# Performance work log

Hardware: AMD Instinct MI355X
Metric: run time of the kernel (lower is better)

## Reference

```python
import jax, jax.numpy as jnp
import numpy as np

N = 100000
E = 1600000
F_IN = 256
HEADS = 8
C1 = 8
NCLS = 16
NEG_SLOPE = 0.2


def setup_inputs() -> dict:
    key = jax.random.key(0)
    ks = jax.random.split(key, 8)
    x = jax.random.normal(ks[0], (N, F_IN), dtype=jnp.float32)
    edge_index = jax.random.randint(ks[1], (2, E), 0, N, dtype=jnp.int64)
    W1 = jax.random.normal(ks[2], (F_IN, HEADS * C1), dtype=jnp.float32) * (1.0 / np.sqrt(F_IN))
    a1_src = jax.random.normal(ks[3], (HEADS, C1), dtype=jnp.float32) * 0.1
    a1_dst = jax.random.normal(ks[4], (HEADS, C1), dtype=jnp.float32) * 0.1
    b1 = jnp.zeros((HEADS * C1,), dtype=jnp.float32)
    W2 = jax.random.normal(ks[5], (HEADS * C1, NCLS), dtype=jnp.float32) * (1.0 / np.sqrt(HEADS * C1))
    a2_src = jax.random.normal(ks[6], (1, NCLS), dtype=jnp.float32) * 0.1
    a2_dst = jax.random.normal(ks[7], (1, NCLS), dtype=jnp.float32) * 0.1
    b2 = jnp.zeros((NCLS,), dtype=jnp.float32)
    return {"x": x, "edge_index": edge_index, "W1": W1, "a1_src": a1_src,
            "a1_dst": a1_dst, "b1": b1, "W2": W2, "a2_src": a2_src,
            "a2_dst": a2_dst, "b2": b2}


def gat_layer(x, src, dst, W, a_src, a_dst, b, heads, out_c, concat):
    n = x.shape[0]
    h = (x @ W).reshape(n, heads, out_c)            # [N,H,C]
    al_src = (h * a_src).sum(-1)                    # [N,H]
    al_dst = (h * a_dst).sum(-1)                    # [N,H]
    e = jax.nn.leaky_relu(al_src[src] + al_dst[dst], NEG_SLOPE)  # [E',H]
    m = jax.ops.segment_max(e, dst, num_segments=n)              # per-dst max
    alpha = jnp.exp(e - m[dst])
    denom = jax.ops.segment_sum(alpha, dst, num_segments=n)
    alpha = alpha / denom[dst]
    out = jax.ops.segment_sum(h[src] * alpha[:, :, None], dst, num_segments=n)  # [N,H,C]
    out = out.reshape(n, heads * out_c) if concat else out.mean(axis=1)
    return out + b


def reference(x, edge_index, W1, a1_src, a1_dst, b1, W2, a2_src, a2_dst, b2):
    # add self-loops (PyG GATConv default)
    loop = jnp.arange(N, dtype=edge_index.dtype)
    src = jnp.concatenate([edge_index[0], loop])
    dst = jnp.concatenate([edge_index[1], loop])
    # dropout layers are identity in eval mode
    h = jax.nn.elu(gat_layer(x, src, dst, W1, a1_src, a1_dst, b1, HEADS, C1, True))
    out = gat_layer(h, src, dst, W2, a2_src, a2_dst, b2, 1, NCLS, False)
    return jax.nn.log_softmax(out, axis=-1)
```

## Files before the change

### kernel.cpp

```cpp
#include <hip/hip_runtime.h>
#include <math.h>

#define NN   100000
#define EE   1600000
#define FIN  256
#define NCLS 16
#define NEG  0.2f

#define NEDGE (EE + NN)
#define WBKT  256
#define NBKT  ((NN + WBKT - 1) / WBKT)
#define CAP   5120
#define ABLK  4096
#define NABLK ((NEDGE + ABLK - 1) / ABLK)
#define NGBLK ((NN + 63) / 64)

#define OFF_GCNT  0
#define OFF_BASE  392
#define OFF_ROW   784
#define OFF_BKT   100788
#define OFF_ADJ   (OFF_BKT + NBKT*CAP)
#define OFF_H1B   (OFF_ADJ + NEDGE)
#define OFF_H1E   (OFF_H1B + NN*32)
#define OFF_AL1S  (OFF_H1E + NN*32)
#define OFF_AL1D  (OFF_AL1S + NN*8)
#define OFF_H2B   (OFF_AL1D + NN*8)
#define OFF_AL2S  (OFF_H2B + NN*8)
#define OFF_AL2D  (OFF_AL2S + NN)

__device__ __forceinline__ float lrelu(float x) { return x >= 0.f ? x : NEG * x; }
__device__ __forceinline__ unsigned short f2bf(float x) {
    unsigned u = __float_as_uint(x);
    return (unsigned short)((u + 0x7FFF + ((u >> 16) & 1)) >> 16);
}
__device__ __forceinline__ float bf2f(unsigned short b) {
    return __uint_as_float(((unsigned)b) << 16);
}
__device__ __forceinline__ float bflo(unsigned u) { return __uint_as_float(u << 16); }
__device__ __forceinline__ float bfhi(unsigned u) { return __uint_as_float(u & 0xFFFF0000u); }

__global__ __launch_bounds__(256) void k_binA_gemm1(
    const int* __restrict__ esrc, const int* __restrict__ edst,
    int* __restrict__ gcnt, unsigned* __restrict__ bkt,
    const float* __restrict__ x, const float* __restrict__ W1,
    const float* __restrict__ a1s, const float* __restrict__ a1d,
    unsigned short* __restrict__ h1b, float* __restrict__ al1s, float* __restrict__ al1d)
{
    const int t = threadIdx.x;
    if (blockIdx.x < NABLK) {
        __shared__ int lcnt[NBKT];
        __shared__ int lbase[NBKT];
        const int e0 = blockIdx.x * ABLK;
        for (int i = t; i < NBKT; i += 256) lcnt[i] = 0;
        __syncthreads();

        unsigned wrd[16];
        unsigned short bb[16], ll[16];
        #pragma unroll
        for (int j = 0; j < 16; ++j) {
            int ei = e0 + j * 256 + t;
            bb[j] = 0xFFFFu;
            if (ei < NEDGE) {
                int s, d;
                if (ei < EE) { s = esrc[ei]; d = edst[ei]; } else { s = d = ei - EE; }
                int b = d >> 8;
                wrd[j] = ((unsigned)s << 8) | (unsigned)(d & 255);
                bb[j] = (unsigned short)b;
                ll[j] = (unsigned short)atomicAdd(&lcnt[b], 1);
            }
        }
        __syncthreads();
        for (int i = t; i < NBKT; i += 256)
            lbase[i] = lcnt[i] ? atomicAdd(&gcnt[i], lcnt[i]) : 0;
        __syncthreads();
        #pragma unroll
        for (int j = 0; j < 16; ++j) {
            if (bb[j] != 0xFFFFu) {
                int b = bb[j];
                bkt[(size_t)b * CAP + lbase[b] + ll[j]] = wrd[j];
            }
        }
        return;
    }

    __shared__ float sxT[32][68];
    __shared__ float sW[32][64];
    const int n0 = (blockIdx.x - NABLK) * 64;
    const int tr = t >> 4, tc = t & 15;

    const int xr0 = t >> 3,         xf0 = t & 7;
    const int xr1 = (t + 256) >> 3, xf1 = (t + 256) & 7;
    const int wr0 = t >> 4,         wf0 = t & 15;
    const int wr1 = (t + 256) >> 4, wf1 = (t + 256) & 15;
    const int nx0 = n0 + xr0, nx1 = n0 + xr1;

    float acc[4][4] = {};
    float4 px0, px1, pw0, pw1;

    px0 = (nx0 < NN) ? *(const float4*)(x + (size_t)nx0 * FIN + xf0 * 4)
                     : make_float4(0.f, 0.f, 0.f, 0.f);
    px1 = (nx1 < NN) ? *(const float4*)(x + (size_t)nx1 * FIN + xf1 * 4)
                     : make_float4(0.f, 0.f, 0.f, 0.f);
    pw0 = *(const float4*)(W1 + (size_t)wr0 * 64 + wf0 * 4);
    pw1 = *(const float4*)(W1 + (size_t)wr1 * 64 + wf1 * 4);

    for (int kc = 0; kc < 256; kc += 32) {
        __syncthreads();
        sxT[xf0 * 4 + 0][xr0] = px0.x;
        sxT[xf0 * 4 + 1][xr0] = px0.y;
        sxT[xf0 * 4 + 2][xr0] = px0.z;
        sxT[xf0 * 4 + 3][xr0] = px0.w;
        sxT[xf1 * 4 + 0][xr1] = px1.x;
        sxT[xf1 * 4 + 1][xr1] = px1.y;
        sxT[xf1 * 4 + 2][xr1] = px1.z;
        sxT[xf1 * 4 + 3][xr1] = px1.w;
        *(float4*)&sW[wr0][wf0 * 4] = pw0;
        *(float4*)&sW[wr1][wf1 * 4] = pw1;
        __syncthreads();

        if (kc + 32 < 256) {
            int kn = kc + 32;
            px0 = (nx0 < NN) ? *(const float4*)(x + (size_t)nx0 * FIN + kn + xf0 * 4)
                             : make_float4(0.f, 0.f, 0.f, 0.f);
            px1 = (nx1 < NN) ? *(const float4*)(x + (size_t)nx1 * FIN + kn + xf1 * 4)
                             : make_float4(0.f, 0.f, 0.f, 0.f);
            pw0 = *(const float4*)(W1 + (size_t)(kn + wr0) * 64 + wf0 * 4);
            pw1 = *(const float4*)(W1 + (size_t)(kn + wr1) * 64 + wf1 * 4);
        }

        #pragma unroll
        for (int k = 0; k < 32; ++k) {
            float4 a = *(const float4*)&sxT[k][tr * 4];
            float4 b = *(const float4*)&sW[k][tc * 4];
            acc[0][0] += a.x * b.x; acc[0][1] += a.x * b.y; acc[0][2] += a.x * b.z; acc[0][3] += a.x * b.w;
            acc[1][0] += a.y * b.x; acc[1][1] += a.y * b.y; acc[1][2] += a.y * b.z; acc[1][3] += a.y * b.w;
            acc[2][0] += a.z * b.x; acc[2][1] += a.z * b.y; acc[2][2] += a.z * b.z; acc[2][3] += a.z * b.w;
            acc[3][0] += a.w * b.x; acc[3][1] += a.w * b.y; acc[3][2] += a.w * b.z; acc[3][3] += a.w * b.w;
        }
    }

    #pragma unroll
    for (int j = 0; j < 4; ++j) {
        int n = n0 + tr * 4 + j;
        if (n < NN) {
            ushort4 v = make_ushort4(f2bf(acc[j][0]), f2bf(acc[j][1]), f2bf(acc[j][2]), f2bf(acc[j][3]));
            *(ushort4*)(h1b + (size_t)n * 64 + tc * 4) = v;
        }
    }

    float sa[4], da[4];
    #pragma unroll
    for (int u = 0; u < 4; ++u) { sa[u] = a1s[tc * 4 + u]; da[u] = a1d[tc * 4 + u]; }
    #pragma unroll
    for (int j = 0; j < 4; ++j) {
        float vs = acc[j][0] * sa[0] + acc[j][1] * sa[1] + acc[j][2] * sa[2] + acc[j][3] * sa[3];
        float vd = acc[j][0] * da[0] + acc[j][1] * da[1] + acc[j][2] * da[2] + acc[j][3] * da[3];
        vs += __shfl_xor(vs, 1, 64);
        vd += __shfl_xor(vd, 1, 64);
        int n = n0 + tr * 4 + j;
        if (!(tc & 1) && n < NN) {
            al1s[n * 8 + (tc >> 1)] = vs;
            al1d[n * 8 + (tc >> 1)] = vd;
        }
    }
}

__global__ __launch_bounds__(512) void k_scanB(
    const int* __restrict__ gcnt, int* __restrict__ base, int* __restrict__ row)
{
    __shared__ int s[512];
    int t = threadIdx.x;
    int v = (t < NBKT) ? gcnt[t] : 0;
    s[t] = v;
    __syncthreads();
    for (int off = 1; off < 512; off <<= 1) {
        int u = (t >= off) ? s[t - off] : 0;
        __syncthreads();
        s[t] += u;
        __syncthreads();
    }
    if (t <= NBKT) base[t] = s[t] - v;
    if (t == 0) row[NN] = NEDGE;
}

__global__ __launch_bounds__(256) void k_binC(
    const int* __restrict__ gcnt, const int* __restrict__ base,
    const unsigned* __restrict__ bkt, int* __restrict__ row, int* __restrict__ adj)
{
    __shared__ unsigned wd[CAP];
    __shared__ int hist[256], pref[256], cnt2[256];
    const int g = blockIdx.x, t = threadIdx.x;
    const int cn = gcnt[g], bs = base[g];
    hist[t] = 0; cnt2[t] = 0;
    __syncthreads();
    for (int i = t; i < cn; i += 256) {
        unsigned w = bkt[(size_t)g * CAP + i];
        wd[i] = w;
        atomicAdd(&hist[w & 255], 1);
    }
    __syncthreads();
    int v = hist[t];
    pref[t] = v;
    __syncthreads();
    for (int off = 1; off < 256; off <<= 1) {
        int u = (t >= off) ? pref[t - off] : 0;
        __syncthreads();
        pref[t] += u;
        __syncthreads();
    }
    int ex = pref[t] - v;
    int n = g * 256 + t;
    if (n < NN) row[n] = bs + ex;
    pref[t] = ex;
    __syncthreads();
    for (int i = t; i < cn; i += 256) {
        unsigned w = wd[i];
        int dl = w & 255;
        int p = atomicAdd(&cnt2[dl], 1);
        adj[bs + pref[dl] + p] = (int)(w >> 8);
    }
}

__global__ __launch_bounds__(256) void k_agg1(
    const int* __restrict__ row, const int* __restrict__ adj,
    const float* __restrict__ al1s, const float* __restrict__ al1d,
    const unsigned* __restrict__ h1b2, const float* __restrict__ b1,
    unsigned* __restrict__ h1e2)
{
    const int wv = threadIdx.x >> 6, lane = threadIdx.x & 63;
    const int n = blockIdx.x * 4 + wv;
    const int q = lane >> 4;
    const int r = lane & 15;
    const int h = r >> 1;
    const float ald = al1d[n * 8 + h];
    const int r0 = row[n], r1 = row[n + 1];

    float dsum = 0.f, ax = 0.f, ay = 0.f, bx = 0.f, by = 0.f;
    for (int c0 = r0; c0 < r1; c0 += 64) {
        int li = c0 + lane;
        int adjv = adj[li < r1 ? li : r0];
        int m = r1 - c0; if (m > 64) m = 64;
        int k = 0;
        for (; k + 16 <= m; k += 16) {
            int s0 = __shfl(adjv, k + 0  + q, 64);
            int s1 = __shfl(adjv, k + 4  + q, 64);
            int s2 = __shfl(adjv, k + 8  + q, 64);
            int s3 = __shfl(adjv, k + 12 + q, 64);
            float a0 = al1s[s0 * 8 + h];
            float a1 = al1s[s1 * 8 + h];
            float a2 = al1s[s2 * 8 + h];
            float a3 = al1s[s3 * 8 + h];
            uint2 u0 = *(const uint2*)(h1b2 + s0 * 32 + r * 2);
            uint2 u1 = *(const uint2*)(h1b2 + s1 * 32 + r * 2);
            uint2 u2 = *(const uint2*)(h1b2 + s2 * 32 + r * 2);
            uint2 u3 = *(const uint2*)(h1b2 + s3 * 32 + r * 2);
            float w0 = __expf(lrelu(a0 + ald));
            float w1 = __expf(lrelu(a1 + ald));
            float w2 = __expf(lrelu(a2 + ald));
            float w3 = __expf(lrelu(a3 + ald));
            dsum += (w0 + w1) + (w2 + w3);
            ax += w0 * bflo(u0.x) + w1 * bflo(u1.x) + w2 * bflo(u2.x) + w3 * bflo(u3.x);
            ay += w0 * bfhi(u0.x) + w1 * bfhi(u1.x) + w2 * bfhi(u2.x) + w3 * bfhi(u3.x);
            bx += w0 * bflo(u0.y) + w1 * bflo(u1.y) + w2 * bflo(u2.y) + w3 * bflo(u3.y);
            by += w0 * bfhi(u0.y) + w1 * bfhi(u1.y) + w2 * bfhi(u2.y) + w3 * bfhi(u3.y);
        }
        for (; k < m; k += 4) {
            int kk = k + q;
            bool act = kk < m;
            int s0 = __shfl(adjv, act ? kk : 0, 64);
            float w0 = act ? __expf(lrelu(al1s[s0 * 8 + h] + ald)) : 0.f;
            uint2 u0 = *(const uint2*)(h1b2 + s0 * 32 + r * 2);
            dsum += w0;
            ax += w0 * bflo(u0.x);
            ay += w0 * bfhi(u0.x);
            bx += w0 * bflo(u0.y);
            by += w0 * bfhi(u0.y);
        }
    }
    dsum += __shfl_xor(dsum, 16, 64); dsum += __shfl_xor(dsum, 32, 64);
    ax   += __shfl_xor(ax,   16, 64); ax   += __shfl_xor(ax,   32, 64);
    ay   += __shfl_xor(ay,   16, 64); ay   += __shfl_xor(ay,   32, 64);
    bx   += __shfl_xor(bx,   16, 64); bx   += __shfl_xor(bx,   32, 64);
    by   += __shfl_xor(by,   16, 64); by   += __shfl_xor(by,   32, 64);

    float inv = 1.f / dsum;
    float v0 = ax * inv + b1[r * 4 + 0];
    float v1 = ay * inv + b1[r * 4 + 1];
    float v2 = bx * inv + b1[r * 4 + 2];
    float v3 = by * inv + b1[r * 4 + 3];
    v0 = v0 > 0.f ? v0 : __expf(v0) - 1.f;
    v1 = v1 > 0.f ? v1 : __expf(v1) - 1.f;
    v2 = v2 > 0.f ? v2 : __expf(v2) - 1.f;
    v3 = v3 > 0.f ? v3 : __expf(v3) - 1.f;
    if (q == 0) {
        uint2 o;
        o.x = (unsigned)f2bf(v0) | ((unsigned)f2bf(v1) << 16);
        o.y = (unsigned)f2bf(v2) | ((unsigned)f2bf(v3) << 16);
        *(uint2*)(h1e2 + n * 32 + r * 2) = o;
    }
}

__global__ __launch_bounds__(256) void k_gemm2(
    const unsigned short* __restrict__ h1e, const float* __restrict__ W2,
    const float* __restrict__ a2s, const float* __restrict__ a2d,
    unsigned short* __restrict__ h2b, float* __restrict__ al2s, float* __restrict__ al2d)
{
    __shared__ float sW[64 * 16];
    const int t = threadIdx.x;
    for (int i = t; i < 64 * 16; i += 256) sW[i] = W2[i];
    __syncthreads();
    const int n = blockIdx.x * 16 + (t >> 4);
    const int k = t & 15;
    if (n >= NN) return;
    const unsigned short* hr = h1e + (size_t)n * 64;
    float acc = 0.f;
    #pragma unroll
    for (int c = 0; c < 64; ++c) acc += bf2f(hr[c]) * sW[c * 16 + k];
    h2b[(size_t)n * 16 + k] = f2bf(acc);
    float vs = acc * a2s[k], vd = acc * a2d[k];
    #pragma unroll
    for (int off = 1; off < 16; off <<= 1) {
        vs += __shfl_xor(vs, off, 64);
        vd += __shfl_xor(vd, off, 64);
    }
    if (k == 0) { al2s[n] = vs; al2d[n] = vd; }
}

__global__ __launch_bounds__(256) void k_agg2(
    const int* __restrict__ row, const int* __restrict__ adj,
    const float* __restrict__ al2s, const float* __restrict__ al2d,
    const unsigned* __restrict__ h2b2, const float* __restrict__ b2,
    float* __restrict__ out)
{
    const int wv = threadIdx.x >> 6, lane = threadIdx.x & 63;
    const int n = blockIdx.x * 4 + wv;
    const float ald = al2d[n];
    const int r0 = row[n], r1 = row[n + 1];

    const int j = lane >> 2;
    const int r = lane & 3;
    float dsum = 0.f, ax = 0.f, ay = 0.f, bx = 0.f, by = 0.f;
    for (int i = r0; i < r1; i += 16) {
        int i0 = i + j;
        bool act = i0 < r1;
        int s = adj[act ? i0 : r0];
        float w = act ? __expf(lrelu(al2s[s] + ald)) : 0.f;
        uint2 u = *(const uint2*)(h2b2 + s * 8 + r * 2);
        dsum += w;
        ax += w * bflo(u.x);
        ay += w * bfhi(u.x);
        bx += w * bflo(u.y);
        by += w * bfhi(u.y);
    }
    #pragma unroll
    for (int off = 4; off < 64; off <<= 1) {
        dsum += __shfl_xor(dsum, off, 64);
        ax   += __shfl_xor(ax,   off, 64);
        ay   += __shfl_xor(ay,   off, 64);
        bx   += __shfl_xor(bx,   off, 64);
        by   += __shfl_xor(by,   off, 64);
    }
    float inv = 1.f / dsum;
    float v0 = ax * inv + b2[r * 4 + 0];
    float v1 = ay * inv + b2[r * 4 + 1];
    float v2 = bx * inv + b2[r * 4 + 2];
    float v3 = by * inv + b2[r * 4 + 3];

    float mx = fmaxf(fmaxf(v0, v1), fmaxf(v2, v3));
    mx = fmaxf(mx, __shfl_xor(mx, 1, 64));
    mx = fmaxf(mx, __shfl_xor(mx, 2, 64));
    float se = __expf(v0 - mx) + __expf(v1 - mx) + __expf(v2 - mx) + __expf(v3 - mx);
    se += __shfl_xor(se, 1, 64);
    se += __shfl_xor(se, 2, 64);
    float ls = mx + __logf(se);
    if (j == 0)
        *(float4*)(out + (size_t)n * 16 + r * 4) = make_float4(v0 - ls, v1 - ls, v2 - ls, v3 - ls);
}

extern "C" void kernel_launch(void* const* d_in, const int* in_sizes, int n_in,
                              void* d_out, int out_size, void* d_ws, size_t ws_size,
                              hipStream_t stream)
{
    const float* x    = (const float*)d_in[0];
    const int*   eidx = (const int*)d_in[1];
    const float* W1   = (const float*)d_in[2];
    const float* a1s  = (const float*)d_in[3];
    const float* a1d  = (const float*)d_in[4];
    const float* b1   = (const float*)d_in[5];
    const float* W2   = (const float*)d_in[6];
    const float* a2s  = (const float*)d_in[7];
    const float* a2d  = (const float*)d_in[8];
    const float* b2   = (const float*)d_in[9];
    float* out = (float*)d_out;
    float* ws  = (float*)d_ws;

    const int* esrc = eidx;
    const int* edst = eidx + EE;

    int* gcnt = (int*)(ws + OFF_GCNT);
    int* base = (int*)(ws + OFF_BASE);
    int* row  = (int*)(ws + OFF_ROW);
    unsigned* bkt = (unsigned*)(ws + OFF_BKT);
    int* adj  = (int*)(ws + OFF_ADJ);
    unsigned short* h1b = (unsigned short*)(ws + OFF_H1B);
    unsigned short* h1e = (unsigned short*)(ws + OFF_H1E);
    float* al1s  = ws + OFF_AL1S;
    float* al1d  = ws + OFF_AL1D;
    unsigned short* h2b = (unsigned short*)(ws + OFF_H2B);
    float* al2s  = ws + OFF_AL2S;
    float* al2d  = ws + OFF_AL2D;

    hipMemsetAsync(gcnt, 0, 392 * sizeof(int), stream);

    k_binA_gemm1<<<NABLK + NGBLK, 256, 0, stream>>>(esrc, edst, gcnt, bkt,
                                                    x, W1, a1s, a1d, h1b, al1s, al1d);
    k_scanB<<<1,    512, 0, stream>>>(gcnt, base, row);
    k_binC <<<NBKT, 256, 0, stream>>>(gcnt, base, bkt, row, adj);

    k_agg1 <<<NN / 4, 256, 0, stream>>>(row, adj, al1s, al1d, (const unsigned*)h1b, b1, (unsigned*)h1e);
    k_gemm2<<<NN / 16, 256, 0, stream>>>(h1e, W2, a2s, a2d, h2b, al2s, al2d);
    k_agg2 <<<NN / 4, 256, 0, stream>>>(row, adj, al2s, al2d, (const unsigned*)h2b, b2, out);
}
```

Measured before the change: 355.3 us.

## Split gemm1 blocks across binning kernels and stage gemm2 inputs in LDS

The layer-1 GEMM blocks are split so that some run alongside the edge-binning pass (binA) and the rest alongside the CSR build pass (binC). This balances work across the two launches and fills the GPU while binC's few large blocks run. Shared memory is now a raw buffer shared between the fused bodies. gemm2 also loads each 16-node tile of bf16 features into LDS with coalesced uint2 reads and unpacks two values per word, replacing strided per-thread short loads. The larger LDS footprint in the fused binC kernel may lower occupancy for the gemm blocks it hosts.

Measured after the change: 361.4 us. No clear change (+1.7%).

```diff
diff --git a/kernel.cpp b/kernel.cpp
--- a/kernel.cpp
+++ b/kernel.cpp
@@ -14,6 +14,8 @@
 #define ABLK  4096
 #define NABLK ((NEDGE + ABLK - 1) / ABLK)
 #define NGBLK ((NN + 63) / 64)
+#define NG1   576
+#define NG2   (NGBLK - NG1)
 
 #define OFF_GCNT  0
 #define OFF_BASE  392
@@ -39,53 +41,15 @@
 __device__ __forceinline__ float bflo(unsigned u) { return __uint_as_float(u << 16); }
 __device__ __forceinline__ float bfhi(unsigned u) { return __uint_as_float(u & 0xFFFF0000u); }
 
-__global__ __launch_bounds__(256) void k_binA_gemm1(
-    const int* __restrict__ esrc, const int* __restrict__ edst,
-    int* __restrict__ gcnt, unsigned* __restrict__ bkt,
+
+__device__ __forceinline__ void gemm1_body(
+    char* smem, int n0, int t,
     const float* __restrict__ x, const float* __restrict__ W1,
     const float* __restrict__ a1s, const float* __restrict__ a1d,
     unsigned short* __restrict__ h1b, float* __restrict__ al1s, float* __restrict__ al1d)
 {
-    const int t = threadIdx.x;
-    if (blockIdx.x < NABLK) {
-        __shared__ int lcnt[NBKT];
-        __shared__ int lbase[NBKT];
-        const int e0 = blockIdx.x * ABLK;
-        for (int i = t; i < NBKT; i += 256) lcnt[i] = 0;
-        __syncthreads();
-
-        unsigned wrd[16];
-        unsigned short bb[16], ll[16];
-        #pragma unroll
-        for (int j = 0; j < 16; ++j) {
-            int ei = e0 + j * 256 + t;
-            bb[j] = 0xFFFFu;
-            if (ei < NEDGE) {
-                int s, d;
-                if (ei < EE) { s = esrc[ei]; d = edst[ei]; } else { s = d = ei - EE; }
-                int b = d >> 8;
-                wrd[j] = ((unsigned)s << 8) | (unsigned)(d & 255);
-                bb[j] = (unsigned short)b;
-                ll[j] = (unsigned short)atomicAdd(&lcnt[b], 1);
-            }
-        }
-        __syncthreads();
-        for (int i = t; i < NBKT; i += 256)
-            lbase[i] = lcnt[i] ? atomicAdd(&gcnt[i], lcnt[i]) : 0;
-        __syncthreads();
-        #pragma unroll
-        for (int j = 0; j < 16; ++j) {
-            if (bb[j] != 0xFFFFu) {
-                int b = bb[j];
-                bkt[(size_t)b * CAP + lbase[b] + ll[j]] = wrd[j];
-            }
-        }
-        return;
-    }
-
-    __shared__ float sxT[32][68];
-    __shared__ float sW[32][64];
-    const int n0 = (blockIdx.x - NABLK) * 64;
+    float (*sxT)[68] = (float(*)[68])smem;
+    float (*sW)[64]  = (float(*)[64])(smem + 32 * 68 * 4);
     const int tr = t >> 4, tc = t & 15;
 
     const int xr0 = t >> 3,         xf0 = t & 7;
@@ -165,31 +129,54 @@
     }
 }
 
-__global__ __launch_bounds__(512) void k_scanB(
-    const int* __restrict__ gcnt, int* __restrict__ base, int* __restrict__ row)
-{
-    __shared__ int s[512];
-    int t = threadIdx.x;
-    int v = (t < NBKT) ? gcnt[t] : 0;
-    s[t] = v;
-    __syncthreads();
-    for (int off = 1; off < 512; off <<= 1) {
-        int u = (t >= off) ? s[t - off] : 0;
-        __syncthreads();
-        s[t] += u;
-        __syncthreads();
-    }
-    if (t <= NBKT) base[t] = s[t] - v;
-    if (t == 0) row[NN] = NEDGE;
-}
-
-__global__ __launch_bounds__(256) void k_binC(
+__device__ __forceinline__ void binA_body(
+    char* smem, int blk, int t,
+    const int* __restrict__ esrc, const int* __restrict__ edst,
+    int* __restrict__ gcnt, unsigned* __restrict__ bkt)
+{
+    int* lcnt  = (int*)smem;
+    int* lbase = lcnt + NBKT;
+    const int e0 = blk * ABLK;
+    for (int i = t; i < NBKT; i += 256) lcnt[i] = 0;
+    __syncthreads();
+
+    unsigned wrd[16];
+    unsigned short bb[16], ll[16];
+    #pragma unroll
+    for (int j = 0; j < 16; ++j) {
+        int ei = e0 + j * 256 + t;
+        bb[j] = 0xFFFFu;
+        if (ei < NEDGE) {
+            int s, d;
+            if (ei < EE) { s = esrc[ei]; d = edst[ei]; } else { s = d = ei - EE; }
+            int b = d >> 8;
+            wrd[j] = ((unsigned)s << 8) | (unsigned)(d & 255);
+            bb[j] = (unsigned short)b;
+            ll[j] = (unsigned short)atomicAdd(&lcnt[b], 1);
+        }
+    }
+    __syncthreads();
+    for (int i = t; i < NBKT; i += 256)
+        lbase[i] = lcnt[i] ? atomicAdd(&gcnt[i], lcnt[i]) : 0;
+    __syncthreads();
+    #pragma unroll
+    for (int j = 0; j < 16; ++j) {
+        if (bb[j] != 0xFFFFu) {
+            int b = bb[j];
+            bkt[(size_t)b * CAP + lbase[b] + ll[j]] = wrd[j];
+        }
+    }
+}
+
+__device__ __forceinline__ void binC_body(
+    char* smem, int g, int t,
     const int* __restrict__ gcnt, const int* __restrict__ base,
     const unsigned* __restrict__ bkt, int* __restrict__ row, int* __restrict__ adj)
 {
-    __shared__ unsigned wd[CAP];
-    __shared__ int hist[256], pref[256], cnt2[256];
-    const int g = blockIdx.x, t = threadIdx.x;
+    unsigned* wd = (unsigned*)smem;
+    int* hist = (int*)(smem + CAP * 4);
+    int* pref = hist + 256;
+    int* cnt2 = pref + 256;
     const int cn = gcnt[g], bs = base[g];
     hist[t] = 0; cnt2[t] = 0;
     __syncthreads();
@@ -219,6 +206,55 @@
         int p = atomicAdd(&cnt2[dl], 1);
         adj[bs + pref[dl] + p] = (int)(w >> 8);
     }
+}
+
+
+__global__ __launch_bounds__(256) void k_binA_gemm1(
+    const int* __restrict__ esrc, const int* __restrict__ edst,
+    int* __restrict__ gcnt, unsigned* __restrict__ bkt,
+    const float* __restrict__ x, const float* __restrict__ W1,
+    const float* __restrict__ a1s, const float* __restrict__ a1d,
+    unsigned short* __restrict__ h1b, float* __restrict__ al1s, float* __restrict__ al1d)
+{
+    __shared__ __align__(16) char smem[16896];
+    const int t = threadIdx.x;
+    if (blockIdx.x < NABLK)
+        binA_body(smem, blockIdx.x, t, esrc, edst, gcnt, bkt);
+    else
+        gemm1_body(smem, (blockIdx.x - NABLK) * 64, t, x, W1, a1s, a1d, h1b, al1s, al1d);
+}
+
+__global__ __launch_bounds__(256) void k_binC_gemm1(
+    const int* __restrict__ gcnt, const int* __restrict__ base,
+    const unsigned* __restrict__ bkt, int* __restrict__ row, int* __restrict__ adj,
+    const float* __restrict__ x, const float* __restrict__ W1,
+    const float* __restrict__ a1s, const float* __restrict__ a1d,
+    unsigned short* __restrict__ h1b, float* __restrict__ al1s, float* __restrict__ al1d)
+{
+    __shared__ __align__(16) char smem[23552];
+    const int t = threadIdx.x;
+    if (blockIdx.x < NBKT)
+        binC_body(smem, blockIdx.x, t, gcnt, base, bkt, row, adj);
+    else
+        gemm1_body(smem, (NG1 + (int)blockIdx.x - NBKT) * 64, t, x, W1, a1s, a1d, h1b, al1s, al1d);
+}
+
+__global__ __launch_bounds__(512) void k_scanB(
+    const int* __restrict__ gcnt, int* __restrict__ base, int* __restrict__ row)
+{
+    __shared__ int s[512];
+    int t = threadIdx.x;
+    int v = (t < NBKT) ? gcnt[t] : 0;
+    s[t] = v;
+    __syncthreads();
+    for (int off = 1; off < 512; off <<= 1) {
+        int u = (t >= off) ? s[t - off] : 0;
+        __syncthreads();
+        s[t] += u;
+        __syncthreads();
+    }
+    if (t <= NBKT) base[t] = s[t] - v;
+    if (t == 0) row[NN] = NEDGE;
 }
 
 __global__ __launch_bounds__(256) void k_agg1(
@@ -301,21 +337,32 @@
 }
 
 __global__ __launch_bounds__(256) void k_gemm2(
-    const unsigned short* __restrict__ h1e, const float* __restrict__ W2,
+    const unsigned* __restrict__ h1e2, const float* __restrict__ W2,
     const float* __restrict__ a2s, const float* __restrict__ a2d,
     unsigned short* __restrict__ h2b, float* __restrict__ al2s, float* __restrict__ al2d)
 {
     __shared__ float sW[64 * 16];
+    __shared__ unsigned sh[16][33];
     const int t = threadIdx.x;
     for (int i = t; i < 64 * 16; i += 256) sW[i] = W2[i];
-    __syncthreads();
-    const int n = blockIdx.x * 16 + (t >> 4);
-    const int k = t & 15;
-    if (n >= NN) return;
-    const unsigned short* hr = h1e + (size_t)n * 64;
+    const int nb = blockIdx.x * 16;
+    {
+        int idx = t * 2;
+        int rrow = idx >> 5, rcol = idx & 31;
+        uint2 v = *(const uint2*)(h1e2 + (size_t)(nb + rrow) * 32 + rcol);
+        sh[rrow][rcol]     = v.x;
+        sh[rrow][rcol + 1] = v.y;
+    }
+    __syncthreads();
+    const int ln = t >> 4;
+    const int k  = t & 15;
+    const int n  = nb + ln;
     float acc = 0.f;
     #pragma unroll
-    for (int c = 0; c < 64; ++c) acc += bf2f(hr[c]) * sW[c * 16 + k];
+    for (int c2 = 0; c2 < 32; ++c2) {
+        unsigned u = sh[ln][c2];
+        acc += bflo(u) * sW[(c2 * 2) * 16 + k] + bfhi(u) * sW[(c2 * 2 + 1) * 16 + k];
+    }
     h2b[(size_t)n * 16 + k] = f2bf(acc);
     float vs = acc * a2s[k], vd = acc * a2d[k];
     #pragma unroll
@@ -412,12 +459,13 @@
 
     hipMemsetAsync(gcnt, 0, 392 * sizeof(int), stream);
 
-    k_binA_gemm1<<<NABLK + NGBLK, 256, 0, stream>>>(esrc, edst, gcnt, bkt,
-                                                    x, W1, a1s, a1d, h1b, al1s, al1d);
-    k_scanB<<<1,    512, 0, stream>>>(gcnt, base, row);
-    k_binC <<<NBKT, 256, 0, stream>>>(gcnt, base, bkt, row, adj);
+    k_binA_gemm1<<<NABLK + NG1, 256, 0, stream>>>(esrc, edst, gcnt, bkt,
+                                                  x, W1, a1s, a1d, h1b, al1s, al1d);
+    k_scanB<<<1, 512, 0, stream>>>(gcnt, base, row);
+    k_binC_gemm1<<<NBKT + NG2, 256, 0, stream>>>(gcnt, base, bkt, row, adj,
+                                                 x, W1, a1s, a1d, h1b, al1s, al1d);
 
     k_agg1 <<<NN / 4, 256, 0, stream>>>(row, adj, al1s, al1d, (const unsigned*)h1b, b1, (unsigned*)h1e);
-    k_gemm2<<<NN / 16, 256, 0, stream>>>(h1e, W2, a2s, a2d, h2b, al2s, al2d);
+    k_gemm2<<<NN / 16, 256, 0, stream>>>((const unsigned*)h1e, W2, a2s, a2d, h2b, al2s, al2d);
     k_agg2 <<<NN / 4, 256, 0, stream>>>(row, adj, al2s, al2d, (const unsigned*)h2b, b2, out);
 }
```

## Fuse layer-2 GEMM into layer-1 aggregation and share LDS in binning kernel

Applied to the files above, without the earlier changes.

The layer-2 projection (64x16 GEMM plus attention-logit dot products) now runs inside k_agg1's epilogue, using a padded W2 copy in shared memory and wave shuffles. This removes the h1e bf16 round trip through global memory and one kernel launch. The combined binning/GEMM1 kernel now uses a single shared-memory buffer for both block roles, which lowers its LDS footprint and may raise occupancy. In exchange, every agg1 block has to load W2 into LDS and run extra shuffle reductions, and h1 is no longer rounded to bf16 before the second GEMM.

Result: no change. 355.6 us (+0.1%).

```diff
diff --git a/kernel.cpp b/kernel.cpp
--- a/kernel.cpp
+++ b/kernel.cpp
@@ -39,53 +39,15 @@
 __device__ __forceinline__ float bflo(unsigned u) { return __uint_as_float(u << 16); }
 __device__ __forceinline__ float bfhi(unsigned u) { return __uint_as_float(u & 0xFFFF0000u); }
 
-__global__ __launch_bounds__(256) void k_binA_gemm1(
-    const int* __restrict__ esrc, const int* __restrict__ edst,
-    int* __restrict__ gcnt, unsigned* __restrict__ bkt,
+
+__device__ __forceinline__ void gemm1_body(
+    char* smem, int n0, int t,
     const float* __restrict__ x, const float* __restrict__ W1,
     const float* __restrict__ a1s, const float* __restrict__ a1d,
     unsigned short* __restrict__ h1b, float* __restrict__ al1s, float* __restrict__ al1d)
 {
-    const int t = threadIdx.x;
-    if (blockIdx.x < NABLK) {
-        __shared__ int lcnt[NBKT];
-        __shared__ int lbase[NBKT];
-        const int e0 = blockIdx.x * ABLK;
-        for (int i = t; i < NBKT; i += 256) lcnt[i] = 0;
-        __syncthreads();
-
-        unsigned wrd[16];
-        unsigned short bb[16], ll[16];
-        #pragma unroll
-        for (int j = 0; j < 16; ++j) {
-            int ei = e0 + j * 256 + t;
-            bb[j] = 0xFFFFu;
-            if (ei < NEDGE) {
-                int s, d;
-                if (ei < EE) { s = esrc[ei]; d = edst[ei]; } else { s = d = ei - EE; }
-                int b = d >> 8;
-                wrd[j] = ((unsigned)s << 8) | (unsigned)(d & 255);
-                bb[j] = (unsigned short)b;
-                ll[j] = (unsigned short)atomicAdd(&lcnt[b], 1);
-            }
-        }
-        __syncthreads();
-        for (int i = t; i < NBKT; i += 256)
-            lbase[i] = lcnt[i] ? atomicAdd(&gcnt[i], lcnt[i]) : 0;
-        __syncthreads();
-        #pragma unroll
-        for (int j = 0; j < 16; ++j) {
-            if (bb[j] != 0xFFFFu) {
-                int b = bb[j];
-                bkt[(size_t)b * CAP + lbase[b] + ll[j]] = wrd[j];
-            }
-        }
-        return;
-    }
-
-    __shared__ float sxT[32][68];
-    __shared__ float sW[32][64];
-    const int n0 = (blockIdx.x - NABLK) * 64;
+    float (*sxT)[68] = (float(*)[68])smem;
+    float (*sW)[64]  = (float(*)[64])(smem + 32 * 68 * 4);
     const int tr = t >> 4, tc = t & 15;
 
     const int xr0 = t >> 3,         xf0 = t & 7;
@@ -165,6 +127,60 @@
     }
 }
 
+__device__ __forceinline__ void binA_body(
+    char* smem, int blk, int t,
+    const int* __restrict__ esrc, const int* __restrict__ edst,
+    int* __restrict__ gcnt, unsigned* __restrict__ bkt)
+{
+    int* lcnt  = (int*)smem;
+    int* lbase = lcnt + NBKT;
+    const int e0 = blk * ABLK;
+    for (int i = t; i < NBKT; i += 256) lcnt[i] = 0;
+    __syncthreads();
+
+    unsigned wrd[16];
+    unsigned short bb[16], ll[16];
+    #pragma unroll
+    for (int j = 0; j < 16; ++j) {
+        int ei = e0 + j * 256 + t;
+        bb[j] = 0xFFFFu;
+        if (ei < NEDGE) {
+            int s, d;
+            if (ei < EE) { s = esrc[ei]; d = edst[ei]; } else { s = d = ei - EE; }
+            int b = d >> 8;
+            wrd[j] = ((unsigned)s << 8) | (unsigned)(d & 255);
+            bb[j] = (unsigned short)b;
+            ll[j] = (unsigned short)atomicAdd(&lcnt[b], 1);
+        }
+    }
+    __syncthreads();
+    for (int i = t; i < NBKT; i += 256)
+        lbase[i] = lcnt[i] ? atomicAdd(&gcnt[i], lcnt[i]) : 0;
+    __syncthreads();
+    #pragma unroll
+    for (int j = 0; j < 16; ++j) {
+        if (bb[j] != 0xFFFFu) {
+            int b = bb[j];
+            bkt[(size_t)b * CAP + lbase[b] + ll[j]] = wrd[j];
+        }
+    }
+}
+
+__global__ __launch_bounds__(256) void k_binA_gemm1(
+    const int* __restrict__ esrc, const int* __restrict__ edst,
+    int* __restrict__ gcnt, unsigned* __restrict__ bkt,
+    const float* __restrict__ x, const float* __restrict__ W1,
+    const float* __restrict__ a1s, const float* __restrict__ a1d,
+    unsigned short* __restrict__ h1b, float* __restrict__ al1s, float* __restrict__ al1d)
+{
+    __shared__ __align__(16) char smem[16896];
+    const int t = threadIdx.x;
+    if (blockIdx.x < NABLK)
+        binA_body(smem, blockIdx.x, t, esrc, edst, gcnt, bkt);
+    else
+        gemm1_body(smem, (blockIdx.x - NABLK) * 64, t, x, W1, a1s, a1d, h1b, al1s, al1d);
+}
+
 __global__ __launch_bounds__(512) void k_scanB(
     const int* __restrict__ gcnt, int* __restrict__ base, int* __restrict__ row)
 {
@@ -225,9 +241,15 @@
     const int* __restrict__ row, const int* __restrict__ adj,
     const float* __restrict__ al1s, const float* __restrict__ al1d,
     const unsigned* __restrict__ h1b2, const float* __restrict__ b1,
-    unsigned* __restrict__ h1e2)
-{
-    const int wv = threadIdx.x >> 6, lane = threadIdx.x & 63;
+    const float* __restrict__ W2, const float* __restrict__ a2s, const float* __restrict__ a2d,
+    unsigned short* __restrict__ h2b, float* __restrict__ al2s, float* __restrict__ al2d)
+{
+    __shared__ float sW2[64 * 17];
+    const int t = threadIdx.x;
+    for (int i = t; i < 64 * 16; i += 256) sW2[(i >> 4) * 17 + (i & 15)] = W2[i];
+    __syncthreads();
+
+    const int wv = t >> 6, lane = t & 63;
     const int n = blockIdx.x * 4 + wv;
     const int q = lane >> 4;
     const int r = lane & 15;
@@ -292,38 +314,35 @@
     v1 = v1 > 0.f ? v1 : __expf(v1) - 1.f;
     v2 = v2 > 0.f ? v2 : __expf(v2) - 1.f;
     v3 = v3 > 0.f ? v3 : __expf(v3) - 1.f;
-    if (q == 0) {
-        uint2 o;
-        o.x = (unsigned)f2bf(v0) | ((unsigned)f2bf(v1) << 16);
-        o.y = (unsigned)f2bf(v2) | ((unsigned)f2bf(v3) << 16);
-        *(uint2*)(h1e2 + n * 32 + r * 2) = o;
-    }
-}
-
-__global__ __launch_bounds__(256) void k_gemm2(
-    const unsigned short* __restrict__ h1e, const float* __restrict__ W2,
-    const float* __restrict__ a2s, const float* __restrict__ a2d,
-    unsigned short* __restrict__ h2b, float* __restrict__ al2s, float* __restrict__ al2d)
-{
-    __shared__ float sW[64 * 16];
-    const int t = threadIdx.x;
-    for (int i = t; i < 64 * 16; i += 256) sW[i] = W2[i];
-    __syncthreads();
-    const int n = blockIdx.x * 16 + (t >> 4);
-    const int k = t & 15;
-    if (n >= NN) return;
-    const unsigned short* hr = h1e + (size_t)n * 64;
-    float acc = 0.f;
-    #pragma unroll
-    for (int c = 0; c < 64; ++c) acc += bf2f(hr[c]) * sW[c * 16 + k];
-    h2b[(size_t)n * 16 + k] = f2bf(acc);
-    float vs = acc * a2s[k], vd = acc * a2d[k];
+
+    const int kb = q * 4;
+    float p0 = 0.f, p1 = 0.f, p2 = 0.f, p3 = 0.f;
+    {
+        const float* wrow0 = &sW2[(r * 4 + 0) * 17 + kb];
+        const float* wrow1 = &sW2[(r * 4 + 1) * 17 + kb];
+        const float* wrow2 = &sW2[(r * 4 + 2) * 17 + kb];
+        const float* wrow3 = &sW2[(r * 4 + 3) * 17 + kb];
+        p0 = v0 * wrow0[0] + v1 * wrow1[0] + v2 * wrow2[0] + v3 * wrow3[0];
+        p1 = v0 * wrow0[1] + v1 * wrow1[1] + v2 * wrow2[1] + v3 * wrow3[1];
+        p2 = v0 * wrow0[2] + v1 * wrow1[2] + v2 * wrow2[2] + v3 * wrow3[2];
+        p3 = v0 * wrow0[3] + v1 * wrow1[3] + v2 * wrow2[3] + v3 * wrow3[3];
+    }
     #pragma unroll
     for (int off = 1; off < 16; off <<= 1) {
-        vs += __shfl_xor(vs, off, 64);
-        vd += __shfl_xor(vd, off, 64);
-    }
-    if (k == 0) { al2s[n] = vs; al2d[n] = vd; }
+        p0 += __shfl_xor(p0, off, 64);
+        p1 += __shfl_xor(p1, off, 64);
+        p2 += __shfl_xor(p2, off, 64);
+        p3 += __shfl_xor(p3, off, 64);
+    }
+    if (r == 0) {
+        ushort4 o = make_ushort4(f2bf(p0), f2bf(p1), f2bf(p2), f2bf(p3));
+        *(ushort4*)(h2b + (size_t)n * 16 + kb) = o;
+    }
+    float vs = p0 * a2s[kb] + p1 * a2s[kb + 1] + p2 * a2s[kb + 2] + p3 * a2s[kb + 3];
+    float vd = p0 * a2d[kb] + p1 * a2d[kb + 1] + p2 * a2d[kb + 2] + p3 * a2d[kb + 3];
+    vs += __shfl_xor(vs, 16, 64); vs += __shfl_xor(vs, 32, 64);
+    vd += __shfl_xor(vd, 16, 64); vd += __shfl_xor(vd, 32, 64);
+    if (lane == 0) { al2s[n] = vs; al2d[n] = vd; }
 }
 
 __global__ __launch_bounds__(256) void k_agg2(
@@ -403,7 +422,6 @@
     unsigned* bkt = (unsigned*)(ws + OFF_BKT);
     int* adj  = (int*)(ws + OFF_ADJ);
     unsigned short* h1b = (unsigned short*)(ws + OFF_H1B);
-    unsigned short* h1e = (unsigned short*)(ws + OFF_H1E);
     float* al1s  = ws + OFF_AL1S;
     float* al1d  = ws + OFF_AL1D;
     unsigned short* h2b = (unsigned short*)(ws + OFF_H2B);
@@ -417,7 +435,7 @@
     k_scanB<<<1,    512, 0, stream>>>(gcnt, base, row);
     k_binC <<<NBKT, 256, 0, stream>>>(gcnt, base, bkt, row, adj);
 
-    k_agg1 <<<NN / 4, 256, 0, stream>>>(row, adj, al1s, al1d, (const unsigned*)h1b, b1, (unsigned*)h1e);
-    k_gemm2<<<NN / 16, 256, 0, stream>>>(h1e, W2, a2s, a2d, h2b, al2s, al2d);
+    k_agg1 <<<NN / 4, 256, 0, stream>>>(row, adj, al1s, al1d, (const unsigned*)h1b, b1,
+                                        W2, a2s, a2d, h2b, al2s, al2d);
     k_agg2 <<<NN / 4, 256, 0, stream>>>(row, adj, al2s, al2d, (const unsigned*)h2b, b2, out);
 }
```
